# Performance work log

Measured on AMD Instinct MI355X. Metric: run time of the kernel, lower is better.

The kernel has to match this reference:

```python
import jax, jax.numpy as jnp
import numpy as np
from math import sqrt

B, S, E, H = 4, 4096, 512, 64


def setup_inputs() -> dict:
    key = jax.random.key(0)
    ks = jax.random.split(key, 9)
    std = sqrt(2.0 / (E + 4 * H))
    x_query = jax.random.normal(ks[0], (B, S, E), dtype=jnp.float32)
    x_key = jax.random.normal(ks[1], (B, S, E), dtype=jnp.float32)
    x_value = jax.random.normal(ks[2], (B, S, E), dtype=jnp.float32)
    Wq = jax.random.normal(ks[3], (E, H), dtype=jnp.float32) * std
    Wk = jax.random.normal(ks[4], (E, H), dtype=jnp.float32) * std
    Wv = jax.random.normal(ks[5], (E, H), dtype=jnp.float32) * std
    bq = jnp.zeros((H,), dtype=jnp.float32)
    bk = jnp.zeros((H,), dtype=jnp.float32)
    bv = jnp.zeros((H,), dtype=jnp.float32)
    # causal mask: True entries are masked out (set to -inf), as in scores[mask] = -inf
    mask = jnp.broadcast_to(jnp.triu(jnp.ones((S, S), dtype=bool), k=1), (B, S, S))
    return {"x_query": x_query, "x_key": x_key, "x_value": x_value,
            "Wq": Wq, "bq": bq, "Wk": Wk, "bk": bk, "Wv": Wv, "bv": bv,
            "mask": mask}


def reference(x_query, x_key, x_value, Wq, bq, Wk, bk, Wv, bv, mask):
    scale = 1.0 / sqrt(H)
    Q = x_query @ Wq + bq              # [B, S, H]
    K = x_key @ Wk + bk                # [B, S, H]
    V = x_value @ Wv + bv              # [B, S, H]
    scores = jnp.einsum('bqh,bkh->bqk', Q, K) * scale  # [B, S, S]
    scores = jnp.where(mask, -jnp.inf, scores)
    attn = jax.nn.softmax(scores, axis=-1)
    Z = jnp.einsum('bqk,bkh->bqh', attn, V)             # [B, S, H]
    return Z
```

## Files before the change

kernel.cpp:

```cpp
#include <hip/hip_runtime.h>
#include <math.h>

#define BB 4
#define SS 4096
#define EE 512
#define HH 64
#define NSPLIT 4
#define NQ (BB * SS)

typedef __bf16 bf16x8 __attribute__((ext_vector_type(8)));
typedef short  s16x8  __attribute__((ext_vector_type(8)));
typedef float  f32x4  __attribute__((ext_vector_type(4)));

static __device__ __forceinline__ unsigned short f2bf(float f) {
    union { float f; unsigned int u; } v; v.f = f;
    unsigned int r = v.u + 0x7fffu + ((v.u >> 16) & 1u);
    return (unsigned short)(r >> 16);
}

static __device__ __forceinline__ f32x4 mfma_bf16(s16x8 a, s16x8 b, f32x4 c) {
    return __builtin_amdgcn_mfma_f32_16x16x32_bf16(
        __builtin_bit_cast(bf16x8, a), __builtin_bit_cast(bf16x8, b), c, 0, 0, 0);
}

__global__ __launch_bounds__(256) void qkv_proj_kernel(
    const float* __restrict__ Xq, const float* __restrict__ Xk, const float* __restrict__ Xv,
    const float* __restrict__ Wq, const float* __restrict__ bq,
    const float* __restrict__ Wk, const float* __restrict__ bk,
    const float* __restrict__ Wv, const float* __restrict__ bv,
    unsigned short* __restrict__ Qbf, unsigned short* __restrict__ Kbf,
    unsigned short* __restrict__ Vtb)
{
    const int mtx = blockIdx.y;
    const float* X; const float* W; const float* bias;
    if (mtx == 0)      { X = Xq; W = Wq; bias = bq; }
    else if (mtx == 1) { X = Xk; W = Wk; bias = bk; }
    else               { X = Xv; W = Wv; bias = bv; }

    __shared__ float Xt[16][132];
    __shared__ float Ws[16][68];

    const int tid = threadIdx.x;
    const int tx  = tid & 15;
    const int ty  = tid >> 4;
    const int r0  = blockIdx.x * 128;

    const int srow = tid >> 1;
    const int seh  = (tid & 1) * 8;
    const int we   = tid >> 4;
    const int wc   = tid & 15;

    float acc[8][4];
    #pragma unroll
    for (int i = 0; i < 8; ++i)
        #pragma unroll
        for (int j = 0; j < 4; ++j) acc[i][j] = 0.f;

    for (int e0 = 0; e0 < EE; e0 += 16) {
        const float4 xa  = *(const float4*)&X[(size_t)(r0 + srow) * EE + e0 + seh];
        const float4 xb  = *(const float4*)&X[(size_t)(r0 + srow) * EE + e0 + seh + 4];
        const float4 wv4 = *(const float4*)&W[(size_t)(e0 + we) * HH + wc * 4];
        __syncthreads();
        Xt[seh + 0][srow] = xa.x; Xt[seh + 1][srow] = xa.y;
        Xt[seh + 2][srow] = xa.z; Xt[seh + 3][srow] = xa.w;
        Xt[seh + 4][srow] = xb.x; Xt[seh + 5][srow] = xb.y;
        Xt[seh + 6][srow] = xb.z; Xt[seh + 7][srow] = xb.w;
        *(float4*)&Ws[we][wc * 4] = wv4;
        __syncthreads();

        #pragma unroll
        for (int e = 0; e < 16; ++e) {
            const float4 xr0 = *(const float4*)&Xt[e][ty * 8];
            const float4 xr1 = *(const float4*)&Xt[e][ty * 8 + 4];
            const float4 wr  = *(const float4*)&Ws[e][tx * 4];
            const float xv[8] = {xr0.x, xr0.y, xr0.z, xr0.w, xr1.x, xr1.y, xr1.z, xr1.w};
            const float wv_[4] = {wr.x, wr.y, wr.z, wr.w};
            #pragma unroll
            for (int i = 0; i < 8; ++i)
                #pragma unroll
                for (int j = 0; j < 4; ++j)
                    acc[i][j] = fmaf(xv[i], wv_[j], acc[i][j]);
        }
    }

    const float4 bv4 = *(const float4*)&bias[tx * 4];
    const float bb_[4] = {bv4.x, bv4.y, bv4.z, bv4.w};
    if (mtx < 2) {
        unsigned short* Out = (mtx == 0) ? Qbf : Kbf;
        #pragma unroll
        for (int i = 0; i < 8; ++i) {
            ushort4 o;
            o.x = f2bf(acc[i][0] + bb_[0]);
            o.y = f2bf(acc[i][1] + bb_[1]);
            o.z = f2bf(acc[i][2] + bb_[2]);
            o.w = f2bf(acc[i][3] + bb_[3]);
            *(ushort4*)&Out[(size_t)(r0 + ty * 8 + i) * HH + tx * 4] = o;
        }
    } else {
        const int b  = r0 >> 12;
        const int s0 = (r0 & 4095) + ty * 8;
        #pragma unroll
        for (int j = 0; j < 4; ++j) {
            s16x8 pk;
            #pragma unroll
            for (int i = 0; i < 8; ++i) pk[i] = (short)f2bf(acc[i][j] + bb_[j]);
            *(s16x8*)&Vtb[((size_t)b * HH + tx * 4 + j) * SS + s0] = pk;
        }
    }
}

__global__ __launch_bounds__(256) void attn_partial_kernel(
    const unsigned short* __restrict__ Qbf, const unsigned short* __restrict__ Kbf,
    const unsigned short* __restrict__ Vtb, float* __restrict__ o_part,
    float* __restrict__ m_part, float* __restrict__ l_part)
{
    __shared__ short Ks[32 * 72];
    __shared__ short Vs[64 * 40];
    __shared__ short Pl[4 * 16 * 40];

    const int tid  = threadIdx.x;
    const int b    = blockIdx.z;
    const int c    = blockIdx.y;
    const int qb0  = blockIdx.x * 64;
    const int lane = tid & 63;
    const int w    = tid >> 6;
    const int l15  = lane & 15;
    const int lg   = lane >> 4;
    const int qw0  = qb0 + w * 16;
    const float scale = 0.125f;

    const size_t qrow = (size_t)(b * SS + qw0 + l15) * HH;
    const s16x8 qf0 = *(const s16x8*)&Qbf[qrow + lg * 8];
    const s16x8 qf1 = *(const s16x8*)&Qbf[qrow + 32 + lg * 8];

    f32x4 o0 = {0,0,0,0}, o1 = {0,0,0,0}, o2 = {0,0,0,0}, o3 = {0,0,0,0};
    float m[4], l[4];
    #pragma unroll
    for (int r = 0; r < 4; ++r) { m[r] = -1.0e30f; l[r] = 0.f; }

    const int kkey = tid >> 3, kseg = tid & 7;
    const int vh   = tid >> 2, vseg = tid & 3;
    const unsigned short* Kb = Kbf + (size_t)b * SS * HH;
    const unsigned short* Vb = Vtb + (size_t)b * HH * SS;

    const int T   = 2 * blockIdx.x + 2;
    const int tpc = (T + NSPLIT - 1) / NSPLIT;
    const int t0  = c * tpc;
    const int t1  = min(t0 + tpc, T);
    short* PW = Pl + w * (16 * 40);

    for (int t = t0; t < t1; ++t) {
        const int k0 = t * 32;
        const s16x8 kst = *(const s16x8*)&Kb[(size_t)(k0 + kkey) * HH + kseg * 8];
        const s16x8 vst = *(const s16x8*)&Vb[(size_t)vh * SS + k0 + vseg * 8];
        __syncthreads();
        *(s16x8*)&Ks[kkey * 72 + kseg * 8] = kst;
        *(s16x8*)&Vs[vh * 40 + vseg * 8]   = vst;
        __syncthreads();

        f32x4 sc0 = {0,0,0,0}, sc1 = {0,0,0,0};
        {
            const s16x8 kf00 = *(const s16x8*)&Ks[l15 * 72 + lg * 8];
            const s16x8 kf10 = *(const s16x8*)&Ks[(16 + l15) * 72 + lg * 8];
            sc0 = mfma_bf16(qf0, kf00, sc0);
            sc1 = mfma_bf16(qf0, kf10, sc1);
            const s16x8 kf01 = *(const s16x8*)&Ks[l15 * 72 + 32 + lg * 8];
            const s16x8 kf11 = *(const s16x8*)&Ks[(16 + l15) * 72 + 32 + lg * 8];
            sc0 = mfma_bf16(qf1, kf01, sc0);
            sc1 = mfma_bf16(qf1, kf11, sc1);
        }

        float s0v[4], s1v[4];
        #pragma unroll
        for (int r = 0; r < 4; ++r) { s0v[r] = sc0[r] * scale; s1v[r] = sc1[r] * scale; }
        if (k0 + 31 > qw0) {
            #pragma unroll
            for (int r = 0; r < 4; ++r) {
                const int qr = qw0 + lg * 4 + r;
                s0v[r] = (k0 + l15      <= qr) ? s0v[r] : -3.0e38f;
                s1v[r] = (k0 + 16 + l15 <= qr) ? s1v[r] : -3.0e38f;
            }
        }

        float tm[4];
        #pragma unroll
        for (int r = 0; r < 4; ++r) tm[r] = fmaxf(s0v[r], s1v[r]);
        #pragma unroll
        for (int d = 1; d < 16; d <<= 1)
            #pragma unroll
            for (int r = 0; r < 4; ++r) tm[r] = fmaxf(tm[r], __shfl_xor(tm[r], d));

        float p0[4], p1[4], al[4];
        #pragma unroll
        for (int r = 0; r < 4; ++r) {
            const float mn = fmaxf(m[r], tm[r]);
            al[r] = __expf(m[r] - mn);
            p0[r] = __expf(s0v[r] - mn);
            p1[r] = __expf(s1v[r] - mn);
            l[r]  = l[r] * al[r] + p0[r] + p1[r];
            m[r]  = mn;
        }
        #pragma unroll
        for (int r = 0; r < 4; ++r) {
            o0[r] *= al[r]; o1[r] *= al[r]; o2[r] *= al[r]; o3[r] *= al[r];
        }

        #pragma unroll
        for (int r = 0; r < 4; ++r) {
            PW[(lg * 4 + r) * 40 + l15]      = (short)f2bf(p0[r]);
            PW[(lg * 4 + r) * 40 + 16 + l15] = (short)f2bf(p1[r]);
        }
        const s16x8 pa = *(const s16x8*)&PW[l15 * 40 + lg * 8];
        {
            const s16x8 v0 = *(const s16x8*)&Vs[(0 * 16 + l15) * 40 + lg * 8];
            o0 = mfma_bf16(pa, v0, o0);
            const s16x8 v1 = *(const s16x8*)&Vs[(1 * 16 + l15) * 40 + lg * 8];
            o1 = mfma_bf16(pa, v1, o1);
            const s16x8 v2 = *(const s16x8*)&Vs[(2 * 16 + l15) * 40 + lg * 8];
            o2 = mfma_bf16(pa, v2, o2);
            const s16x8 v3 = *(const s16x8*)&Vs[(3 * 16 + l15) * 40 + lg * 8];
            o3 = mfma_bf16(pa, v3, o3);
        }
    }

    #pragma unroll
    for (int d = 1; d < 16; d <<= 1)
        #pragma unroll
        for (int r = 0; r < 4; ++r) l[r] += __shfl_xor(l[r], d);

    #pragma unroll
    for (int r = 0; r < 4; ++r) {
        const size_t qlin = (size_t)b * SS + qb0 + w * 16 + lg * 4 + r;
        float* Op = o_part + ((size_t)c * NQ + qlin) * HH;
        Op[0 * 16 + l15] = o0[r];
        Op[1 * 16 + l15] = o1[r];
        Op[2 * 16 + l15] = o2[r];
        Op[3 * 16 + l15] = o3[r];
        if (l15 == 0) {
            m_part[(size_t)c * NQ + qlin] = m[r];
            l_part[(size_t)c * NQ + qlin] = l[r];
        }
    }
}

__global__ __launch_bounds__(256) void attn_combine_kernel(
    const float* __restrict__ o_part, const float* __restrict__ m_part,
    const float* __restrict__ l_part, float* __restrict__ O)
{
    const int g = blockIdx.x * 256 + threadIdx.x;
    const size_t qlin = (size_t)(g >> 4);
    const int h0 = (g & 15) * 4;

    float mv[NSPLIT], lv[NSPLIT];
    float M = -INFINITY;
    #pragma unroll
    for (int cc = 0; cc < NSPLIT; ++cc) {
        mv[cc] = m_part[(size_t)cc * NQ + qlin];
        lv[cc] = l_part[(size_t)cc * NQ + qlin];
        M = fmaxf(M, mv[cc]);
    }
    float L = 0.f;
    float4 acc = make_float4(0.f, 0.f, 0.f, 0.f);
    #pragma unroll
    for (int cc = 0; cc < NSPLIT; ++cc) {
        const float wc = __expf(mv[cc] - M);
        L += lv[cc] * wc;
        const float4 oc = *(const float4*)&o_part[((size_t)cc * NQ + qlin) * HH + h0];
        acc.x += wc * oc.x; acc.y += wc * oc.y;
        acc.z += wc * oc.z; acc.w += wc * oc.w;
    }
    const float inv = 1.0f / L;
    acc.x *= inv; acc.y *= inv; acc.z *= inv; acc.w *= inv;
    *(float4*)&O[qlin * HH + h0] = acc;
}

extern "C" void kernel_launch(void* const* d_in, const int* in_sizes, int n_in,
                              void* d_out, int out_size, void* d_ws, size_t ws_size,
                              hipStream_t stream) {
    const float* xq = (const float*)d_in[0];
    const float* xk = (const float*)d_in[1];
    const float* xv = (const float*)d_in[2];
    const float* Wq = (const float*)d_in[3];
    const float* bq = (const float*)d_in[4];
    const float* Wk = (const float*)d_in[5];
    const float* bk = (const float*)d_in[6];
    const float* Wv = (const float*)d_in[7];
    const float* bv = (const float*)d_in[8];

    unsigned short* Qbf = (unsigned short*)d_ws;
    unsigned short* Kbf = Qbf + (size_t)NQ * HH;
    unsigned short* Vtb = Kbf + (size_t)NQ * HH;
    float* o_part = (float*)(Vtb + (size_t)NQ * HH);
    float* m_part = o_part + (size_t)NSPLIT * NQ * HH;
    float* l_part = m_part + (size_t)NSPLIT * NQ;

    dim3 pgrid(NQ / 128, 3);
    qkv_proj_kernel<<<pgrid, 256, 0, stream>>>(xq, xk, xv, Wq, bq, Wk, bk, Wv, bv,
                                               Qbf, Kbf, Vtb);

    dim3 agrid(SS / 64, NSPLIT, BB);
    attn_partial_kernel<<<agrid, 256, 0, stream>>>(Qbf, Kbf, Vtb,
                                                   o_part, m_part, l_part);

    attn_combine_kernel<<<(NQ * 16) / 256, 256, 0, stream>>>(o_part, m_part, l_part,
                                                             (float*)d_out);
}
```

Baseline: 467.0 us.

## Use split-bf16 MFMA for QKV projection and widen attention key tiles

The fp32 FMA projection is replaced by an MFMA GEMM that splits X and W into bf16 high and low parts and uses three cross products to keep near-fp32 accuracy. A new prep kernel splits and transposes the weights into the workspace. The attention kernel now processes 64-key tiles instead of 32, halving the number of barriers and tile loads. The split count rises from 4 to 8, which adds parallelism but doubles the partial-output traffic into the combine kernel.

```diff
diff --git a/kernel.cpp b/kernel.cpp
--- a/kernel.cpp
+++ b/kernel.cpp
@@ -5,7 +5,7 @@
 #define SS 4096
 #define EE 512
 #define HH 64
-#define NSPLIT 4
+#define NSPLIT 8
 #define NQ (BB * SS)
 
 typedef __bf16 bf16x8 __attribute__((ext_vector_type(8)));
@@ -17,94 +17,140 @@
     unsigned int r = v.u + 0x7fffu + ((v.u >> 16) & 1u);
     return (unsigned short)(r >> 16);
 }
+static __device__ __forceinline__ float bf2f(unsigned short h) {
+    union { unsigned int u; float f; } v; v.u = ((unsigned int)h) << 16;
+    return v.f;
+}
+static __device__ __forceinline__ void split_bf(float x, unsigned short& h, unsigned short& l) {
+    h = f2bf(x);
+    l = f2bf(x - bf2f(h));
+}
 
 static __device__ __forceinline__ f32x4 mfma_bf16(s16x8 a, s16x8 b, f32x4 c) {
     return __builtin_amdgcn_mfma_f32_16x16x32_bf16(
         __builtin_bit_cast(bf16x8, a), __builtin_bit_cast(bf16x8, b), c, 0, 0, 0);
 }
 
+__global__ __launch_bounds__(256) void wprep_kernel(
+    const float* __restrict__ Wq, const float* __restrict__ Wk,
+    const float* __restrict__ Wv,
+    unsigned short* __restrict__ WhT, unsigned short* __restrict__ WlT)
+{
+    const int mat = blockIdx.y;
+    const float* W = (mat == 0) ? Wq : ((mat == 1) ? Wk : Wv);
+    const int base = blockIdx.x * 2048;
+    for (int ii = threadIdx.x; ii < 2048; ii += 256) {
+        const int i = base + ii;
+        const int k = i >> 6, n = i & 63;
+        unsigned short h, l;
+        split_bf(W[i], h, l);
+        const size_t o = ((size_t)mat * HH + n) * EE + k;
+        WhT[o] = h; WlT[o] = l;
+    }
+}
+
 __global__ __launch_bounds__(256) void qkv_proj_kernel(
     const float* __restrict__ Xq, const float* __restrict__ Xk, const float* __restrict__ Xv,
-    const float* __restrict__ Wq, const float* __restrict__ bq,
-    const float* __restrict__ Wk, const float* __restrict__ bk,
-    const float* __restrict__ Wv, const float* __restrict__ bv,
+    const float* __restrict__ bq, const float* __restrict__ bk, const float* __restrict__ bv,
+    const unsigned short* __restrict__ WhT, const unsigned short* __restrict__ WlT,
     unsigned short* __restrict__ Qbf, unsigned short* __restrict__ Kbf,
     unsigned short* __restrict__ Vtb)
 {
     const int mtx = blockIdx.y;
-    const float* X; const float* W; const float* bias;
-    if (mtx == 0)      { X = Xq; W = Wq; bias = bq; }
-    else if (mtx == 1) { X = Xk; W = Wk; bias = bk; }
-    else               { X = Xv; W = Wv; bias = bv; }
-
-    __shared__ float Xt[16][132];
-    __shared__ float Ws[16][68];
-
-    const int tid = threadIdx.x;
-    const int tx  = tid & 15;
-    const int ty  = tid >> 4;
-    const int r0  = blockIdx.x * 128;
-
-    const int srow = tid >> 1;
-    const int seh  = (tid & 1) * 8;
-    const int we   = tid >> 4;
-    const int wc   = tid & 15;
-
-    float acc[8][4];
-    #pragma unroll
-    for (int i = 0; i < 8; ++i)
-        #pragma unroll
-        for (int j = 0; j < 4; ++j) acc[i][j] = 0.f;
-
-    for (int e0 = 0; e0 < EE; e0 += 16) {
-        const float4 xa  = *(const float4*)&X[(size_t)(r0 + srow) * EE + e0 + seh];
-        const float4 xb  = *(const float4*)&X[(size_t)(r0 + srow) * EE + e0 + seh + 4];
-        const float4 wv4 = *(const float4*)&W[(size_t)(e0 + we) * HH + wc * 4];
+    const float* X    = (mtx == 0) ? Xq : ((mtx == 1) ? Xk : Xv);
+    const float* bias = (mtx == 0) ? bq : ((mtx == 1) ? bk : bv);
+
+    __shared__ unsigned short Ah[64 * 72], Al[64 * 72];
+    __shared__ unsigned short Bh[64 * 72], Bl[64 * 72];
+
+    const int tid  = threadIdx.x;
+    const int lane = tid & 63;
+    const int w    = tid >> 6;
+    const int l15  = lane & 15;
+    const int lg   = lane >> 4;
+    const int r0   = blockIdx.x * 64;
+
+    const int arow = tid >> 2;
+    const int asg  = tid & 3;
+
+    f32x4 acc[4] = {{0,0,0,0},{0,0,0,0},{0,0,0,0},{0,0,0,0}};
+
+    for (int c = 0; c < EE / 64; ++c) {
+        const float* xp = &X[(size_t)(r0 + arow) * EE + c * 64 + asg * 16];
+        const float4 x0 = ((const float4*)xp)[0];
+        const float4 x1 = ((const float4*)xp)[1];
+        const float4 x2 = ((const float4*)xp)[2];
+        const float4 x3 = ((const float4*)xp)[3];
+        const size_t wb = ((size_t)mtx * HH + arow) * EE + (size_t)c * 64;
+        const s16x8 wh0 = *(const s16x8*)&WhT[wb + asg * 8];
+        const s16x8 wh1 = *(const s16x8*)&WhT[wb + 32 + asg * 8];
+        const s16x8 wl0 = *(const s16x8*)&WlT[wb + asg * 8];
+        const s16x8 wl1 = *(const s16x8*)&WlT[wb + 32 + asg * 8];
         __syncthreads();
-        Xt[seh + 0][srow] = xa.x; Xt[seh + 1][srow] = xa.y;
-        Xt[seh + 2][srow] = xa.z; Xt[seh + 3][srow] = xa.w;
-        Xt[seh + 4][srow] = xb.x; Xt[seh + 5][srow] = xb.y;
-        Xt[seh + 6][srow] = xb.z; Xt[seh + 7][srow] = xb.w;
-        *(float4*)&Ws[we][wc * 4] = wv4;
+
+        const float xs[16] = {x0.x,x0.y,x0.z,x0.w, x1.x,x1.y,x1.z,x1.w,
+                              x2.x,x2.y,x2.z,x2.w, x3.x,x3.y,x3.z,x3.w};
+        s16x8 ha, hb, la, lb;
+        #pragma unroll
+        for (int i = 0; i < 8; ++i) {
+            unsigned short h, l;
+            split_bf(xs[i], h, l);      ha[i] = (short)h; la[i] = (short)l;
+            split_bf(xs[8 + i], h, l);  hb[i] = (short)h; lb[i] = (short)l;
+        }
+        *(s16x8*)&Ah[arow * 72 + asg * 16]     = ha;
+        *(s16x8*)&Ah[arow * 72 + asg * 16 + 8] = hb;
+        *(s16x8*)&Al[arow * 72 + asg * 16]     = la;
+        *(s16x8*)&Al[arow * 72 + asg * 16 + 8] = lb;
+        *(s16x8*)&Bh[arow * 72 + asg * 8]      = wh0;
+        *(s16x8*)&Bh[arow * 72 + 32 + asg * 8] = wh1;
+        *(s16x8*)&Bl[arow * 72 + asg * 8]      = wl0;
+        *(s16x8*)&Bl[arow * 72 + 32 + asg * 8] = wl1;
         __syncthreads();
 
-        #pragma unroll
-        for (int e = 0; e < 16; ++e) {
-            const float4 xr0 = *(const float4*)&Xt[e][ty * 8];
-            const float4 xr1 = *(const float4*)&Xt[e][ty * 8 + 4];
-            const float4 wr  = *(const float4*)&Ws[e][tx * 4];
-            const float xv[8] = {xr0.x, xr0.y, xr0.z, xr0.w, xr1.x, xr1.y, xr1.z, xr1.w};
-            const float wv_[4] = {wr.x, wr.y, wr.z, wr.w};
-            #pragma unroll
-            for (int i = 0; i < 8; ++i)
-                #pragma unroll
-                for (int j = 0; j < 4; ++j)
-                    acc[i][j] = fmaf(xv[i], wv_[j], acc[i][j]);
-        }
-    }
-
-    const float4 bv4 = *(const float4*)&bias[tx * 4];
-    const float bb_[4] = {bv4.x, bv4.y, bv4.z, bv4.w};
+        const int ma = (w * 16 + l15) * 72;
+        const s16x8 a_h0 = *(const s16x8*)&Ah[ma + lg * 8];
+        const s16x8 a_h1 = *(const s16x8*)&Ah[ma + 32 + lg * 8];
+        const s16x8 a_l0 = *(const s16x8*)&Al[ma + lg * 8];
+        const s16x8 a_l1 = *(const s16x8*)&Al[ma + 32 + lg * 8];
+        #pragma unroll
+        for (int f = 0; f < 4; ++f) {
+            const int nb = (f * 16 + l15) * 72;
+            const s16x8 b_h0 = *(const s16x8*)&Bh[nb + lg * 8];
+            const s16x8 b_h1 = *(const s16x8*)&Bh[nb + 32 + lg * 8];
+            const s16x8 b_l0 = *(const s16x8*)&Bl[nb + lg * 8];
+            const s16x8 b_l1 = *(const s16x8*)&Bl[nb + 32 + lg * 8];
+            acc[f] = mfma_bf16(a_h0, b_h0, acc[f]);
+            acc[f] = mfma_bf16(a_h1, b_h1, acc[f]);
+            acc[f] = mfma_bf16(a_l0, b_h0, acc[f]);
+            acc[f] = mfma_bf16(a_l1, b_h1, acc[f]);
+            acc[f] = mfma_bf16(a_h0, b_l0, acc[f]);
+            acc[f] = mfma_bf16(a_h1, b_l1, acc[f]);
+        }
+    }
+
+    float bcol[4];
+    #pragma unroll
+    for (int f = 0; f < 4; ++f) bcol[f] = bias[f * 16 + l15];
+
     if (mtx < 2) {
         unsigned short* Out = (mtx == 0) ? Qbf : Kbf;
         #pragma unroll
-        for (int i = 0; i < 8; ++i) {
-            ushort4 o;
-            o.x = f2bf(acc[i][0] + bb_[0]);
-            o.y = f2bf(acc[i][1] + bb_[1]);
-            o.z = f2bf(acc[i][2] + bb_[2]);
-            o.w = f2bf(acc[i][3] + bb_[3]);
-            *(ushort4*)&Out[(size_t)(r0 + ty * 8 + i) * HH + tx * 4] = o;
-        }
+        for (int f = 0; f < 4; ++f)
+            #pragma unroll
+            for (int r = 0; r < 4; ++r)
+                Out[(size_t)(r0 + w * 16 + lg * 4 + r) * HH + f * 16 + l15] =
+                    f2bf(acc[f][r] + bcol[f]);
     } else {
         const int b  = r0 >> 12;
-        const int s0 = (r0 & 4095) + ty * 8;
-        #pragma unroll
-        for (int j = 0; j < 4; ++j) {
-            s16x8 pk;
-            #pragma unroll
-            for (int i = 0; i < 8; ++i) pk[i] = (short)f2bf(acc[i][j] + bb_[j]);
-            *(s16x8*)&Vtb[((size_t)b * HH + tx * 4 + j) * SS + s0] = pk;
+        const int s0 = (r0 & 4095) + w * 16 + lg * 4;
+        #pragma unroll
+        for (int f = 0; f < 4; ++f) {
+            ushort4 pk;
+            pk.x = f2bf(acc[f][0] + bcol[f]);
+            pk.y = f2bf(acc[f][1] + bcol[f]);
+            pk.z = f2bf(acc[f][2] + bcol[f]);
+            pk.w = f2bf(acc[f][3] + bcol[f]);
+            *(ushort4*)&Vtb[((size_t)b * HH + f * 16 + l15) * SS + s0] = pk;
         }
     }
 }
@@ -114,13 +160,13 @@
     const unsigned short* __restrict__ Vtb, float* __restrict__ o_part,
     float* __restrict__ m_part, float* __restrict__ l_part)
 {
-    __shared__ short Ks[32 * 72];
-    __shared__ short Vs[64 * 40];
-    __shared__ short Pl[4 * 16 * 40];
+    __shared__ unsigned short Ks[64 * 68];
+    __shared__ unsigned short Vs[64 * 68];
+    __shared__ unsigned short Pl[4 * 16 * 68];
 
     const int tid  = threadIdx.x;
     const int b    = blockIdx.z;
-    const int c    = blockIdx.y;
+    const int cch  = blockIdx.y;
     const int qb0  = blockIdx.x * 64;
     const int lane = tid & 63;
     const int w    = tid >> 6;
@@ -133,93 +179,104 @@
     const s16x8 qf0 = *(const s16x8*)&Qbf[qrow + lg * 8];
     const s16x8 qf1 = *(const s16x8*)&Qbf[qrow + 32 + lg * 8];
 
-    f32x4 o0 = {0,0,0,0}, o1 = {0,0,0,0}, o2 = {0,0,0,0}, o3 = {0,0,0,0};
+    f32x4 o[4] = {{0,0,0,0},{0,0,0,0},{0,0,0,0},{0,0,0,0}};
     float m[4], l[4];
     #pragma unroll
     for (int r = 0; r < 4; ++r) { m[r] = -1.0e30f; l[r] = 0.f; }
 
-    const int kkey = tid >> 3, kseg = tid & 7;
-    const int vh   = tid >> 2, vseg = tid & 3;
+    const int kkey = tid >> 2, ksg = tid & 3;
     const unsigned short* Kb = Kbf + (size_t)b * SS * HH;
     const unsigned short* Vb = Vtb + (size_t)b * HH * SS;
 
-    const int T   = 2 * blockIdx.x + 2;
+    const int T   = blockIdx.x + 1;
     const int tpc = (T + NSPLIT - 1) / NSPLIT;
-    const int t0  = c * tpc;
+    const int t0  = cch * tpc;
     const int t1  = min(t0 + tpc, T);
-    short* PW = Pl + w * (16 * 40);
+    unsigned short* PW = Pl + w * (16 * 68);
 
     for (int t = t0; t < t1; ++t) {
-        const int k0 = t * 32;
-        const s16x8 kst = *(const s16x8*)&Kb[(size_t)(k0 + kkey) * HH + kseg * 8];
-        const s16x8 vst = *(const s16x8*)&Vb[(size_t)vh * SS + k0 + vseg * 8];
+        const int k0 = t * 64;
+        const s16x8 ka  = *(const s16x8*)&Kb[(size_t)(k0 + kkey) * HH + ksg * 8];
+        const s16x8 kb2 = *(const s16x8*)&Kb[(size_t)(k0 + kkey) * HH + 32 + ksg * 8];
+        const s16x8 va  = *(const s16x8*)&Vb[(size_t)kkey * SS + k0 + ksg * 8];
+        const s16x8 vb2 = *(const s16x8*)&Vb[(size_t)kkey * SS + k0 + 32 + ksg * 8];
         __syncthreads();
-        *(s16x8*)&Ks[kkey * 72 + kseg * 8] = kst;
-        *(s16x8*)&Vs[vh * 40 + vseg * 8]   = vst;
+        *(s16x8*)&Ks[kkey * 68 + ksg * 8]      = ka;
+        *(s16x8*)&Ks[kkey * 68 + 32 + ksg * 8] = kb2;
+        *(s16x8*)&Vs[kkey * 68 + ksg * 8]      = va;
+        *(s16x8*)&Vs[kkey * 68 + 32 + ksg * 8] = vb2;
         __syncthreads();
 
-        f32x4 sc0 = {0,0,0,0}, sc1 = {0,0,0,0};
-        {
-            const s16x8 kf00 = *(const s16x8*)&Ks[l15 * 72 + lg * 8];
-            const s16x8 kf10 = *(const s16x8*)&Ks[(16 + l15) * 72 + lg * 8];
-            sc0 = mfma_bf16(qf0, kf00, sc0);
-            sc1 = mfma_bf16(qf0, kf10, sc1);
-            const s16x8 kf01 = *(const s16x8*)&Ks[l15 * 72 + 32 + lg * 8];
-            const s16x8 kf11 = *(const s16x8*)&Ks[(16 + l15) * 72 + 32 + lg * 8];
-            sc0 = mfma_bf16(qf1, kf01, sc0);
-            sc1 = mfma_bf16(qf1, kf11, sc1);
-        }
-
-        float s0v[4], s1v[4];
-        #pragma unroll
-        for (int r = 0; r < 4; ++r) { s0v[r] = sc0[r] * scale; s1v[r] = sc1[r] * scale; }
-        if (k0 + 31 > qw0) {
-            #pragma unroll
-            for (int r = 0; r < 4; ++r) {
-                const int qr = qw0 + lg * 4 + r;
-                s0v[r] = (k0 + l15      <= qr) ? s0v[r] : -3.0e38f;
-                s1v[r] = (k0 + 16 + l15 <= qr) ? s1v[r] : -3.0e38f;
-            }
+        f32x4 sc[4];
+        #pragma unroll
+        for (int f = 0; f < 4; ++f) {
+            const int kr = (f * 16 + l15) * 68;
+            const s16x8 kfa = *(const s16x8*)&Ks[kr + lg * 8];
+            const s16x8 kfb = *(const s16x8*)&Ks[kr + 32 + lg * 8];
+            f32x4 z = {0, 0, 0, 0};
+            z = mfma_bf16(qf0, kfa, z);
+            z = mfma_bf16(qf1, kfb, z);
+            sc[f] = z;
+        }
+
+        float sv[4][4];
+        #pragma unroll
+        for (int f = 0; f < 4; ++f)
+            #pragma unroll
+            for (int r = 0; r < 4; ++r) sv[f][r] = sc[f][r] * scale;
+        if (k0 + 63 > qw0) {
+            #pragma unroll
+            for (int f = 0; f < 4; ++f)
+                #pragma unroll
+                for (int r = 0; r < 4; ++r) {
+                    const int qr = qw0 + lg * 4 + r;
+                    if (k0 + f * 16 + l15 > qr) sv[f][r] = -3.0e38f;
+                }
         }
 
         float tm[4];
         #pragma unroll
-        for (int r = 0; r < 4; ++r) tm[r] = fmaxf(s0v[r], s1v[r]);
+        for (int r = 0; r < 4; ++r)
+            tm[r] = fmaxf(fmaxf(sv[0][r], sv[1][r]), fmaxf(sv[2][r], sv[3][r]));
         #pragma unroll
         for (int d = 1; d < 16; d <<= 1)
             #pragma unroll
             for (int r = 0; r < 4; ++r) tm[r] = fmaxf(tm[r], __shfl_xor(tm[r], d));
 
-        float p0[4], p1[4], al[4];
+        float al[4];
         #pragma unroll
         for (int r = 0; r < 4; ++r) {
             const float mn = fmaxf(m[r], tm[r]);
             al[r] = __expf(m[r] - mn);
-            p0[r] = __expf(s0v[r] - mn);
-            p1[r] = __expf(s1v[r] - mn);
-            l[r]  = l[r] * al[r] + p0[r] + p1[r];
             m[r]  = mn;
         }
-        #pragma unroll
-        for (int r = 0; r < 4; ++r) {
-            o0[r] *= al[r]; o1[r] *= al[r]; o2[r] *= al[r]; o3[r] *= al[r];
-        }
-
-        #pragma unroll
-        for (int r = 0; r < 4; ++r) {
-            PW[(lg * 4 + r) * 40 + l15]      = (short)f2bf(p0[r]);
-            PW[(lg * 4 + r) * 40 + 16 + l15] = (short)f2bf(p1[r]);
-        }
-        const s16x8 pa = *(const s16x8*)&PW[l15 * 40 + lg * 8];
-        {
-            const s16x8 v0 = *(const s16x8*)&Vs[(0 * 16 + l15) * 40 + lg * 8];
-            o0 = mfma_bf16(pa, v0, o0);
-            const s16x8 v1 = *(const s16x8*)&Vs[(1 * 16 + l15) * 40 + lg * 8];
-            o1 = mfma_bf16(pa, v1, o1);
-            const s16x8 v2 = *(const s16x8*)&Vs[(2 * 16 + l15) * 40 + lg * 8];
-            o2 = mfma_bf16(pa, v2, o2);
-            const s16x8 v3 = *(const s16x8*)&Vs[(3 * 16 + l15) * 40 + lg * 8];
-            o3 = mfma_bf16(pa, v3, o3);
+        float p[4][4];
+        #pragma unroll
+        for (int f = 0; f < 4; ++f)
+            #pragma unroll
+            for (int r = 0; r < 4; ++r) p[f][r] = __expf(sv[f][r] - m[r]);
+        #pragma unroll
+        for (int r = 0; r < 4; ++r)
+            l[r] = l[r] * al[r] + p[0][r] + p[1][r] + p[2][r] + p[3][r];
+        #pragma unroll
+        for (int f = 0; f < 4; ++f)
+            #pragma unroll
+            for (int r = 0; r < 4; ++r) o[f][r] *= al[r];
+
+        #pragma unroll
+        for (int f = 0; f < 4; ++f)
+            #pragma unroll
+            for (int r = 0; r < 4; ++r)
+                PW[(lg * 4 + r) * 68 + f * 16 + l15] = f2bf(p[f][r]);
+        const s16x8 pa0 = *(const s16x8*)&PW[l15 * 68 + lg * 8];
+        const s16x8 pa1 = *(const s16x8*)&PW[l15 * 68 + 32 + lg * 8];
+        #pragma unroll
+        for (int f = 0; f < 4; ++f) {
+            const int vr = (f * 16 + l15) * 68;
+            const s16x8 vfa = *(const s16x8*)&Vs[vr + lg * 8];
+            const s16x8 vfb = *(const s16x8*)&Vs[vr + 32 + lg * 8];
+            o[f] = mfma_bf16(pa0, vfa, o[f]);
+            o[f] = mfma_bf16(pa1, vfb, o[f]);
         }
     }
 
@@ -231,14 +288,12 @@
     #pragma unroll
     for (int r = 0; r < 4; ++r) {
         const size_t qlin = (size_t)b * SS + qb0 + w * 16 + lg * 4 + r;
-        float* Op = o_part + ((size_t)c * NQ + qlin) * HH;
-        Op[0 * 16 + l15] = o0[r];
-        Op[1 * 16 + l15] = o1[r];
-        Op[2 * 16 + l15] = o2[r];
-        Op[3 * 16 + l15] = o3[r];
+        float* Op = o_part + ((size_t)cch * NQ + qlin) * HH;
+        #pragma unroll
+        for (int f = 0; f < 4; ++f) Op[f * 16 + l15] = o[f][r];
         if (l15 == 0) {
-            m_part[(size_t)c * NQ + qlin] = m[r];
-            l_part[(size_t)c * NQ + qlin] = l[r];
+            m_part[(size_t)cch * NQ + qlin] = m[r];
+            l_part[(size_t)cch * NQ + qlin] = l[r];
         }
     }
 }
@@ -290,18 +345,20 @@
     unsigned short* Qbf = (unsigned short*)d_ws;
     unsigned short* Kbf = Qbf + (size_t)NQ * HH;
     unsigned short* Vtb = Kbf + (size_t)NQ * HH;
-    float* o_part = (float*)(Vtb + (size_t)NQ * HH);
+    unsigned short* WhT = Vtb + (size_t)NQ * HH;
+    unsigned short* WlT = WhT + (size_t)3 * HH * EE;
+    float* o_part = (float*)(WlT + (size_t)3 * HH * EE);
     float* m_part = o_part + (size_t)NSPLIT * NQ * HH;
     float* l_part = m_part + (size_t)NSPLIT * NQ;
 
-    dim3 pgrid(NQ / 128, 3);
-    qkv_proj_kernel<<<pgrid, 256, 0, stream>>>(xq, xk, xv, Wq, bq, Wk, bk, Wv, bv,
-                                               Qbf, Kbf, Vtb);
-
-    dim3 agrid(SS / 64, NSPLIT, BB);
-    attn_partial_kernel<<<agrid, 256, 0, stream>>>(Qbf, Kbf, Vtb,
-                                                   o_part, m_part, l_part);
-
-    attn_combine_kernel<<<(NQ * 16) / 256, 256, 0, stream>>>(o_part, m_part, l_part,
-                                                             (float*)d_out);
-}
+    wprep_kernel<<<dim3(16, 3), 256, 0, stream>>>(Wq, Wk, Wv, WhT, WlT);
+
+    qkv_proj_kernel<<<dim3(NQ / 64, 3), 256, 0, stream>>>(
+        xq, xk, xv, bq, bk, bv, WhT, WlT, Qbf, Kbf, Vtb);
+
+    attn_partial_kernel<<<dim3(SS / 64, NSPLIT, BB), 256, 0, stream>>>(
+        Qbf, Kbf, Vtb, o_part, m_part, l_part);
+
+    attn_combine_kernel<<<(NQ * 16) / 256, 256, 0, stream>>>(
+        o_part, m_part, l_part, (float*)d_out);
+}
```

Result: faster. 443.3 us (-5.1%).
